# Optimization experiments

Hardware: AMD Instinct MI355X
Metric: run time of the kernel (lower is better)

Reference implementation:

```python
import jax, jax.numpy as jnp
import numpy as np

K = 3
PAD = 1
KK = K * K
GROUPS = 32  # min(32, dim) with dim=64
EPS = 1e-5


def _conv(x, w, pad):
    return jax.lax.conv_general_dilated(
        x, w, (1, 1), [(pad, pad), (pad, pad)],
        dimension_numbers=('NCHW', 'OIHW', 'NCHW'))


def _bilinear_gather(x, py, px):
    # x: (B,C,H,W); py,px: (B,KK,H,W) float sampling coords (zero pad outside)
    B, C, H, W = x.shape
    xf = x.reshape(B, C, H * W)
    y0f = jnp.floor(py)
    x0f = jnp.floor(px)
    wy1 = py - y0f  # fractional weights (differentiable path to offsets)
    wx1 = px - x0f
    y0 = y0f.astype(jnp.int32)
    x0 = x0f.astype(jnp.int32)

    def g(yi, xi):
        valid = (yi >= 0) & (yi < H) & (xi >= 0) & (xi < W)
        idx = (jnp.clip(yi, 0, H - 1) * W + jnp.clip(xi, 0, W - 1)).reshape(B, 1, -1)
        v = jnp.take_along_axis(xf, idx, axis=2).reshape(B, C, KK, H, W)
        return v * valid[:, None].astype(x.dtype)

    v00 = g(y0, x0)
    v01 = g(y0, x0 + 1)
    v10 = g(y0 + 1, x0)
    v11 = g(y0 + 1, x0 + 1)
    wy1e = wy1[:, None]
    wx1e = wx1[:, None]
    return (v00 * (1 - wy1e) * (1 - wx1e) + v01 * (1 - wy1e) * wx1e
            + v10 * wy1e * (1 - wx1e) + v11 * wy1e * wx1e)


def _forward(x, w_off1, w_off2, w_mask1, w_mask2, weight, bias, gamma, beta):
    B, C, H, W = x.shape
    # offset branch: 1x1 conv then KxK conv -> (B, 2*KK, H, W)
    off = _conv(_conv(x, w_off1, 0), w_off2, PAD).reshape(B, KK, 2, H, W)
    # mask branch -> sigmoid modulation (B, KK, H, W)
    mask = jax.nn.sigmoid(_conv(_conv(x, w_mask1, 0), w_mask2, PAD))
    # base kernel grid (torchvision deform_conv2d: pairs are (dy, dx) per tap)
    ky = jnp.repeat(jnp.arange(K) - PAD, K).astype(x.dtype)
    kx = jnp.tile(jnp.arange(K) - PAD, K).astype(x.dtype)
    py = off[:, :, 0] + jnp.arange(H, dtype=x.dtype)[None, None, :, None] + ky[None, :, None, None]
    px = off[:, :, 1] + jnp.arange(W, dtype=x.dtype)[None, None, None, :] + kx[None, :, None, None]
    samp = _bilinear_gather(x, py, px)  # (B, C, KK, H, W)
    # depthwise deformable conv: per-channel weight over KK taps, modulated by mask
    out = jnp.einsum('bkhw,ck,bckhw->bchw', mask, weight.reshape(C, KK), samp)
    out = out + bias[None, :, None, None]
    # GroupNorm(32, C)
    g = out.reshape(B, GROUPS, C // GROUPS, H, W)
    mu = g.mean(axis=(2, 3, 4), keepdims=True)
    var = g.var(axis=(2, 3, 4), keepdims=True)
    gn = ((g - mu) * jax.lax.rsqrt(var + EPS)).reshape(B, C, H, W)
    gn = gn * gamma[None, :, None, None] + beta[None, :, None, None]
    return jax.nn.gelu(gn, approximate=False)


def setup_inputs() -> dict:
    key = jax.random.key(0)
    ks = jax.random.split(key, 6)
    B, C, H, W = 4, 64, 128, 128
    x = jax.random.normal(ks[0], (B, C, H, W), dtype=jnp.float32)
    w_off1 = jax.random.normal(ks[1], (C, C, 1, 1), dtype=jnp.float32) * 0.05
    w_off2 = jax.random.normal(ks[2], (2 * KK, C, K, K), dtype=jnp.float32) * 0.02
    w_mask1 = jax.random.normal(ks[3], (C, C, 1, 1), dtype=jnp.float32) * 0.05
    w_mask2 = jax.random.normal(ks[4], (KK, C, K, K), dtype=jnp.float32) * 0.05
    bound = 1.0 / np.sqrt(KK)  # kaiming_uniform(a=1) for (C,1,K,K) -> fan_in=KK
    weight = jax.random.uniform(ks[5], (C, 1, K, K), dtype=jnp.float32,
                                minval=-bound, maxval=bound)
    bias = jnp.zeros((C,), dtype=jnp.float32)
    gamma = jnp.ones((C,), dtype=jnp.float32)
    beta = jnp.zeros((C,), dtype=jnp.float32)
    return {'x': x, 'w_off1': w_off1, 'w_off2': w_off2, 'w_mask1': w_mask1,
            'w_mask2': w_mask2, 'weight': weight, 'bias': bias,
            'gamma': gamma, 'beta': beta}


def reference(x, w_off1, w_off2, w_mask1, w_mask2, weight, bias, gamma, beta):
    return _forward(x, w_off1, w_off2, w_mask1, w_mask2, weight, bias, gamma, beta)
```

## Files before the change

kernel.cpp:

```cpp
#include <hip/hip_runtime.h>
#include <math.h>

#define B_  4
#define C_  64
#define H_  128
#define W_  128
#define HW_ (H_*W_)
#define NPIX_ (B_*HW_)
#define GROUPS_ 32

typedef __attribute__((ext_vector_type(8))) short short8;
typedef __attribute__((ext_vector_type(4))) float f32x4;

__device__ inline short f2bf_rne(float f) {
    unsigned u = __float_as_uint(f);
    unsigned r = (u + 0x7FFFu + ((u >> 16) & 1u)) >> 16;
    return (short)r;
}
__device__ inline float bf2f(short h) {
    return __uint_as_float(((unsigned)(unsigned short)h) << 16);
}
__device__ inline short8 ld8(const short* p) {
    union { uint4 u; short8 s; } c;
    c.u = *(const uint4*)p;
    return c.s;
}

__global__ void k0_prep(const float* __restrict__ w_off1, const float* __restrict__ w_mask1,
                        const float* __restrict__ w_off2, const float* __restrict__ w_mask2,
                        short* __restrict__ wc_hi, short* __restrict__ wc_lo) {
    int i = blockIdx.x * 256 + threadIdx.x;
    if (i >= 32 * 576) return;
    int cout = i / 576;
    int r    = i % 576;
    int pos  = r >> 6, ci = r & 63;
    float s = 0.f;
    if (cout < 18) {
        for (int cm = 0; cm < 64; cm++)
            s += w_off2[(cout * 64 + cm) * 9 + pos] * w_off1[cm * 64 + ci];
    } else if (cout < 27) {
        for (int cm = 0; cm < 64; cm++)
            s += w_mask2[((cout - 18) * 64 + cm) * 9 + pos] * w_mask1[cm * 64 + ci];
    }
    short h = f2bf_rne(s);
    wc_hi[i] = h;
    wc_lo[i] = f2bf_rne(s - bf2f(h));
}

__global__ __launch_bounds__(256) void k1_trans(const float* __restrict__ x,
                                                short* __restrict__ xtb) {
    int l   = threadIdx.x & 63;
    int wv  = threadIdx.x >> 6;
    int row = l >> 4, col = l & 15;
    int p0  = blockIdx.x * 64 + wv * 16;
    int b   = p0 >> 14;
    int hw  = p0 & (HW_ - 1);
    const float* xb = x + (size_t)b * C_ * HW_ + hw;
#pragma unroll
    for (int kb = 0; kb < 2; kb++) {
        int ci0 = kb * 32 + row * 8;
        float xv[8];
#pragma unroll
        for (int j = 0; j < 8; j++) xv[j] = xb[(ci0 + j) * HW_ + col];
        short8 a;
#pragma unroll
        for (int j = 0; j < 8; j++) a[j] = f2bf_rne(xv[j]);
        union { short8 s; uint4 u; } cv; cv.s = a;
        *(uint4*)(xtb + ((size_t)(p0 + col)) * 64 + ci0) = cv.u;
    }
}

__global__ __launch_bounds__(256, 2) void k2_mfma(const short* __restrict__ xtb,
                                                  const short* __restrict__ wc_hi,
                                                  const short* __restrict__ wc_lo,
                                                  float* __restrict__ offmask) {
    int l   = threadIdx.x & 63;
    int wv  = threadIdx.x >> 6;
    int row = l >> 4, col = l & 15;
    int blk = blockIdx.x;
    int h   = blk & 127;
    int pb  = blk * 128 + wv * 32;
    int w0  = (pb & 127);

    const short8 zero = {0,0,0,0,0,0,0,0};
    f32x4 a00 = {0.f,0.f,0.f,0.f};
    f32x4 a01 = {0.f,0.f,0.f,0.f};
    f32x4 a10 = {0.f,0.f,0.f,0.f};
    f32x4 a11 = {0.f,0.f,0.f,0.f};

    short8 cw0, cw1, cw2, cw3, ca0, ca1;
    {
        const int kb = 0, pos = 0, dy = -1, dx = -1;
        int ci0 = (kb & 1) * 32 + row * 8;
        int ko  = pos * 64 + ci0;
        cw0 = ld8(wc_hi + (size_t)col * 576 + ko);
        cw1 = ld8(wc_lo + (size_t)col * 576 + ko);
        cw2 = ld8(wc_hi + (size_t)(col + 16) * 576 + ko);
        cw3 = ld8(wc_lo + (size_t)(col + 16) * 576 + ko);
#pragma unroll
        for (int mt = 0; mt < 2; mt++) {
            int pbase = pb + mt * 16 + col;
            int w = w0 + mt * 16 + col;
            bool valid = ((unsigned)(h + dy) < 128u) && ((unsigned)(w + dx) < 128u);
            int addr = valid ? (pbase + dy * 128 + dx) : pbase;
            short8 v = ld8(xtb + (size_t)addr * 64 + ci0);
            if (mt == 0) ca0 = valid ? v : zero; else ca1 = valid ? v : zero;
        }
    }

#pragma unroll
    for (int kb = 0; kb < 18; kb++) {
        short8 nw0, nw1, nw2, nw3, na0, na1;
        if (kb < 17) {
            const int kn = kb + 1;
            const int pos = kn >> 1;
            const int dy = pos / 3 - 1, dx = pos % 3 - 1;
            int ci0 = (kn & 1) * 32 + row * 8;
            int ko  = pos * 64 + ci0;
            nw0 = ld8(wc_hi + (size_t)col * 576 + ko);
            nw1 = ld8(wc_lo + (size_t)col * 576 + ko);
            nw2 = ld8(wc_hi + (size_t)(col + 16) * 576 + ko);
            nw3 = ld8(wc_lo + (size_t)(col + 16) * 576 + ko);
#pragma unroll
            for (int mt = 0; mt < 2; mt++) {
                int pbase = pb + mt * 16 + col;
                int w = w0 + mt * 16 + col;
                bool valid = ((unsigned)(h + dy) < 128u) && ((unsigned)(w + dx) < 128u);
                int addr = valid ? (pbase + dy * 128 + dx) : pbase;
                short8 v = ld8(xtb + (size_t)addr * 64 + ci0);
                if (mt == 0) na0 = valid ? v : zero; else na1 = valid ? v : zero;
            }
        }
        a00 = __builtin_amdgcn_mfma_f32_16x16x32_bf16(ca0, cw0, a00, 0, 0, 0);
        a00 = __builtin_amdgcn_mfma_f32_16x16x32_bf16(ca0, cw1, a00, 0, 0, 0);
        a01 = __builtin_amdgcn_mfma_f32_16x16x32_bf16(ca0, cw2, a01, 0, 0, 0);
        a01 = __builtin_amdgcn_mfma_f32_16x16x32_bf16(ca0, cw3, a01, 0, 0, 0);
        a10 = __builtin_amdgcn_mfma_f32_16x16x32_bf16(ca1, cw0, a10, 0, 0, 0);
        a10 = __builtin_amdgcn_mfma_f32_16x16x32_bf16(ca1, cw1, a10, 0, 0, 0);
        a11 = __builtin_amdgcn_mfma_f32_16x16x32_bf16(ca1, cw2, a11, 0, 0, 0);
        a11 = __builtin_amdgcn_mfma_f32_16x16x32_bf16(ca1, cw3, a11, 0, 0, 0);
        cw0 = nw0; cw1 = nw1; cw2 = nw2; cw3 = nw3;
        ca0 = na0; ca1 = na1;
    }

#pragma unroll
    for (int mt = 0; mt < 2; mt++) {
        f32x4 n0 = mt ? a10 : a00;
        f32x4 n1 = mt ? a11 : a01;
#pragma unroll
        for (int r = 0; r < 4; r++) {
            int p = pb + mt * 16 + row * 4 + r;
            float* om = offmask + (size_t)p * 32;
            om[col] = n0[r];
            if (col < 2)       om[16 + col] = n1[r];
            else if (col < 11) om[16 + col] = 1.f / (1.f + expf(-n1[r]));
        }
    }
}

__global__ __launch_bounds__(256) void k3_deform(const short* __restrict__ xtb,
                                                 const float* __restrict__ offmask,
                                                 const float* __restrict__ weight,
                                                 const float* __restrict__ bias,
                                                 float* __restrict__ out_pre) {
    __shared__ float wl[C_ * 9];
    __shared__ float bl[C_];
    for (int i = threadIdx.x; i < C_ * 9; i += 256) wl[i] = weight[i];
    if (threadIdx.x < C_) bl[threadIdx.x] = bias[threadIdx.x];
    __syncthreads();

    int blk   = blockIdx.x;
    int xcd   = blk & 7;
    int slot  = blk >> 3;
    int b     = slot >> 5;
    int r     = (slot & 31) >> 1;
    int hrow  = slot & 1;
    int h     = xcd * 16 + r;
    int pl    = threadIdx.x >> 2;
    int chunk = threadIdx.x & 3;
    int c0    = chunk * 16;
    int w     = hrow * 64 + pl;
    int hw    = h * W_ + w;
    int P     = b * HW_ + hw;

    float acc[16];
#pragma unroll
    for (int i = 0; i < 16; i++) acc[i] = 0.f;

    const float* po = offmask + (size_t)P * 32;
    const short* xb = xtb + (size_t)b * HW_ * 64;

    for (int k = 0; k < 9; k++) {
        float offy = po[2 * k];
        float offx = po[2 * k + 1];
        float mk   = po[18 + k];
        float py = offy + (float)h + (float)(k / 3 - 1);
        float px = offx + (float)w + (float)(k % 3 - 1);
        float y0f = floorf(py), x0f = floorf(px);
        int y0 = (int)y0f, x0 = (int)x0f;
        int y1 = y0 + 1,   x1 = x0 + 1;
        float wy1 = py - y0f, wx1 = px - x0f;
        float wy0 = 1.f - wy1, wx0 = 1.f - wx1;
        bool vy0 = ((unsigned)y0 < (unsigned)H_);
        bool vy1 = ((unsigned)y1 < (unsigned)H_);
        bool vx0 = ((unsigned)x0 < (unsigned)W_);
        bool vx1 = ((unsigned)x1 < (unsigned)W_);
        int cy0 = min(max(y0, 0), H_ - 1);
        int cy1 = min(max(y1, 0), H_ - 1);
        int cx0 = min(max(x0, 0), W_ - 1);
        int cx1 = min(max(x1, 0), W_ - 1);
        float b00 = wy0 * wx0 * ((vy0 && vx0) ? mk : 0.f);
        float b01 = wy0 * wx1 * ((vy0 && vx1) ? mk : 0.f);
        float b10 = wy1 * wx0 * ((vy1 && vx0) ? mk : 0.f);
        float b11 = wy1 * wx1 * ((vy1 && vx1) ? mk : 0.f);

        const short* p00 = xb + ((size_t)cy0 * W_ + cx0) * 64 + c0;
        const short* p01 = xb + ((size_t)cy0 * W_ + cx1) * 64 + c0;
        const short* p10 = xb + ((size_t)cy1 * W_ + cx0) * 64 + c0;
        const short* p11 = xb + ((size_t)cy1 * W_ + cx1) * 64 + c0;

#pragma unroll
        for (int half = 0; half < 2; half++) {
            uint4 u00 = *(const uint4*)(p00 + 8 * half);
            uint4 u01 = *(const uint4*)(p01 + 8 * half);
            uint4 u10 = *(const uint4*)(p10 + 8 * half);
            uint4 u11 = *(const uint4*)(p11 + 8 * half);
            unsigned a00[4] = {u00.x, u00.y, u00.z, u00.w};
            unsigned a01[4] = {u01.x, u01.y, u01.z, u01.w};
            unsigned a10[4] = {u10.x, u10.y, u10.z, u10.w};
            unsigned a11[4] = {u11.x, u11.y, u11.z, u11.w};
#pragma unroll
            for (int d = 0; d < 4; d++) {
                float s_lo = b00 * __uint_as_float(a00[d] << 16)
                           + b01 * __uint_as_float(a01[d] << 16)
                           + b10 * __uint_as_float(a10[d] << 16)
                           + b11 * __uint_as_float(a11[d] << 16);
                float s_hi = b00 * __uint_as_float(a00[d] & 0xFFFF0000u)
                           + b01 * __uint_as_float(a01[d] & 0xFFFF0000u)
                           + b10 * __uint_as_float(a10[d] & 0xFFFF0000u)
                           + b11 * __uint_as_float(a11[d] & 0xFFFF0000u);
                int c = 8 * half + 2 * d;
                acc[c]     += wl[(c0 + c) * 9 + k] * s_lo;
                acc[c + 1] += wl[(c0 + c + 1) * 9 + k] * s_hi;
            }
        }
    }

    float* op = out_pre + ((size_t)b * C_ + c0) * HW_ + hw;
#pragma unroll
    for (int c = 0; c < 16; c++) op[c * HW_] = acc[c] + bl[c0 + c];
}

__global__ __launch_bounds__(1024) void k4_stats(const float* __restrict__ out_pre,
                                                 float* __restrict__ stats) {
    int bg = blockIdx.x;
    const float4* p = (const float4*)(out_pre + (size_t)bg * 2 * HW_);
    float s = 0.f, ss = 0.f;
    for (int i = threadIdx.x; i < 2 * HW_ / 4; i += 1024) {
        float4 v = p[i];
        s  += v.x + v.y + v.z + v.w;
        ss += v.x * v.x + v.y * v.y + v.z * v.z + v.w * v.w;
    }
#pragma unroll
    for (int m = 1; m < 64; m <<= 1) {
        s  += __shfl_xor(s, m);
        ss += __shfl_xor(ss, m);
    }
    __shared__ float ls[32];
    int lane = threadIdx.x & 63, wid = threadIdx.x >> 6;
    if (lane == 0) { ls[wid] = s; ls[16 + wid] = ss; }
    __syncthreads();
    if (threadIdx.x == 0) {
        float S = 0.f, SS = 0.f;
#pragma unroll
        for (int i = 0; i < 16; i++) { S += ls[i]; SS += ls[16 + i]; }
        const float inv = 1.f / (2.f * HW_);
        float mean = S * inv;
        float var  = SS * inv - mean * mean;
        stats[bg * 2]     = mean;
        stats[bg * 2 + 1] = rsqrtf(var + 1e-5f);
    }
}

__global__ __launch_bounds__(256) void k5_norm_gelu(const float* __restrict__ out_pre,
                                                    const float* __restrict__ stats,
                                                    const float* __restrict__ gamma,
                                                    const float* __restrict__ beta,
                                                    float* __restrict__ out) {
    int i = blockIdx.x * 256 + threadIdx.x;
    int e = i << 2;
    int c = (e >> 14) & (C_ - 1);
    int b = e >> 20;
    int bg = b * GROUPS_ + (c >> 1);
    float mean = stats[bg * 2];
    float rstd = stats[bg * 2 + 1];
    float ga = gamma[c] * rstd;
    float be = beta[c] - mean * ga;
    float4 v = ((const float4*)out_pre)[i];
    float4 r;
    float t;
    t = v.x * ga + be; r.x = 0.5f * t * (1.f + erff(t * 0.70710678118654752f));
    t = v.y * ga + be; r.y = 0.5f * t * (1.f + erff(t * 0.70710678118654752f));
    t = v.z * ga + be; r.z = 0.5f * t * (1.f + erff(t * 0.70710678118654752f));
    t = v.w * ga + be; r.w = 0.5f * t * (1.f + erff(t * 0.70710678118654752f));
    ((float4*)out)[i] = r;
}

extern "C" void kernel_launch(void* const* d_in, const int* in_sizes, int n_in,
                              void* d_out, int out_size, void* d_ws, size_t ws_size,
                              hipStream_t stream) {
    const float* x       = (const float*)d_in[0];
    const float* w_off1  = (const float*)d_in[1];
    const float* w_off2  = (const float*)d_in[2];
    const float* w_mask1 = (const float*)d_in[3];
    const float* w_mask2 = (const float*)d_in[4];
    const float* weight  = (const float*)d_in[5];
    const float* bias    = (const float*)d_in[6];
    const float* gamma   = (const float*)d_in[7];
    const float* beta    = (const float*)d_in[8];
    float* out = (float*)d_out;

    char* ws = (char*)d_ws;
    size_t o = 0;
    short* wc_hi = (short*)(ws + o); o += 32 * 576 * 2;
    short* wc_lo = (short*)(ws + o); o += 32 * 576 * 2;
    o = (o + 255) & ~(size_t)255;
    short* xtb     = (short*)(ws + o); o += (size_t)NPIX_ * 64 * 2;
    float* offmask = (float*)(ws + o); o += (size_t)NPIX_ * 32 * 4;
    float* out_pre = (float*)(ws + o); o += (size_t)NPIX_ * 64 * 4;
    float* stats   = (float*)(ws + o); o += 256 * 4;

    hipLaunchKernelGGL(k0_prep, dim3(72), dim3(256), 0, stream,
                       w_off1, w_mask1, w_off2, w_mask2, wc_hi, wc_lo);
    hipLaunchKernelGGL(k1_trans, dim3(NPIX_ / 64), dim3(256), 0, stream,
                       x, xtb);
    hipLaunchKernelGGL(k2_mfma, dim3(NPIX_ / 128), dim3(256), 0, stream,
                       xtb, wc_hi, wc_lo, offmask);
    hipLaunchKernelGGL(k3_deform, dim3(NPIX_ / 64), dim3(256), 0, stream,
                       xtb, offmask, weight, bias, out_pre);
    hipLaunchKernelGGL(k4_stats, dim3(B_ * GROUPS_), dim3(1024), 0, stream,
                       out_pre, stats);
    hipLaunchKernelGGL(k5_norm_gelu, dim3(NPIX_ * 64 / 4 / 256), dim3(256), 0, stream,
                       out_pre, stats, gamma, beta, out);
}
```

Measured before the change: 149.4 us.

## Fuse GroupNorm partial stats into deform kernel and store intermediate as bf16

The deformable-conv kernel now computes per-group sum and sum-of-squares partials through wavefront shuffles and LDS, so the stats kernel only reduces 256 partials per group instead of rereading the whole fp32 intermediate. The pre-norm intermediate is stored as bf16, which halves its write traffic and the read in the norm/GELU kernel, and that kernel now handles eight elements per thread. The cost is extra reduction work and a block barrier in the deform kernel, plus bf16 rounding of the pre-norm values before normalization, which may loosen accuracy.

```diff
diff --git a/kernel.cpp b/kernel.cpp
--- a/kernel.cpp
+++ b/kernel.cpp
@@ -90,8 +90,8 @@
 
     short8 cw0, cw1, cw2, cw3, ca0, ca1;
     {
-        const int kb = 0, pos = 0, dy = -1, dx = -1;
-        int ci0 = (kb & 1) * 32 + row * 8;
+        const int pos = 0, dy = -1, dx = -1;
+        int ci0 = row * 8;
         int ko  = pos * 64 + ci0;
         cw0 = ld8(wc_hi + (size_t)col * 576 + ko);
         cw1 = ld8(wc_lo + (size_t)col * 576 + ko);
@@ -162,9 +162,12 @@
                                                  const float* __restrict__ offmask,
                                                  const float* __restrict__ weight,
                                                  const float* __restrict__ bias,
-                                                 float* __restrict__ out_pre) {
+                                                 unsigned short* __restrict__ out_pre,
+                                                 float* __restrict__ partials) {
     __shared__ float wl[C_ * 9];
     __shared__ float bl[C_];
+    __shared__ float lds_s[4][4][8];
+    __shared__ float lds_ss[4][4][8];
     for (int i = threadIdx.x; i < C_ * 9; i += 256) wl[i] = weight[i];
     if (threadIdx.x < C_) bl[threadIdx.x] = bias[threadIdx.x];
     __syncthreads();
@@ -182,6 +185,7 @@
     int w     = hrow * 64 + pl;
     int hw    = h * W_ + w;
     int P     = b * HW_ + hw;
+    int slot_img = xcd * 32 + (slot & 31);
 
     float acc[16];
 #pragma unroll
@@ -246,34 +250,64 @@
         }
     }
 
-    float* op = out_pre + ((size_t)b * C_ + c0) * HW_ + hw;
-#pragma unroll
-    for (int c = 0; c < 16; c++) op[c * HW_] = acc[c] + bl[c0 + c];
-}
-
-__global__ __launch_bounds__(1024) void k4_stats(const float* __restrict__ out_pre,
+    unsigned short* op = out_pre + ((size_t)b * C_ + c0) * HW_ + hw;
+#pragma unroll
+    for (int c = 0; c < 16; c++) {
+        acc[c] += bl[c0 + c];
+        op[c * HW_] = (unsigned short)f2bf_rne(acc[c]);
+    }
+
+    float s8[8], ss8[8];
+#pragma unroll
+    for (int j = 0; j < 8; j++) {
+        float a0 = acc[2 * j], a1 = acc[2 * j + 1];
+        s8[j]  = a0 + a1;
+        ss8[j] = a0 * a0 + a1 * a1;
+    }
+#pragma unroll
+    for (int m = 4; m < 64; m <<= 1) {
+#pragma unroll
+        for (int j = 0; j < 8; j++) {
+            s8[j]  += __shfl_xor(s8[j], m);
+            ss8[j] += __shfl_xor(ss8[j], m);
+        }
+    }
+    int lane = threadIdx.x & 63, wid = threadIdx.x >> 6;
+    if (lane < 4) {
+#pragma unroll
+        for (int j = 0; j < 8; j++) {
+            lds_s[wid][lane][j]  = s8[j];
+            lds_ss[wid][lane][j] = ss8[j];
+        }
+    }
+    __syncthreads();
+    if (threadIdx.x < 32) {
+        int g = threadIdx.x;
+        int ch = g >> 3, j = g & 7;
+        float S  = lds_s[0][ch][j] + lds_s[1][ch][j] + lds_s[2][ch][j] + lds_s[3][ch][j];
+        float SS = lds_ss[0][ch][j] + lds_ss[1][ch][j] + lds_ss[2][ch][j] + lds_ss[3][ch][j];
+        float2 v = make_float2(S, SS);
+        *(float2*)(partials + (((size_t)(b * GROUPS_ + g)) * 256 + slot_img) * 2) = v;
+    }
+}
+
+__global__ __launch_bounds__(256) void k4_reduce(const float* __restrict__ partials,
                                                  float* __restrict__ stats) {
     int bg = blockIdx.x;
-    const float4* p = (const float4*)(out_pre + (size_t)bg * 2 * HW_);
-    float s = 0.f, ss = 0.f;
-    for (int i = threadIdx.x; i < 2 * HW_ / 4; i += 1024) {
-        float4 v = p[i];
-        s  += v.x + v.y + v.z + v.w;
-        ss += v.x * v.x + v.y * v.y + v.z * v.z + v.w * v.w;
-    }
+    float2 v = ((const float2*)partials)[bg * 256 + threadIdx.x];
+    float s = v.x, ss = v.y;
 #pragma unroll
     for (int m = 1; m < 64; m <<= 1) {
         s  += __shfl_xor(s, m);
         ss += __shfl_xor(ss, m);
     }
-    __shared__ float ls[32];
+    __shared__ float ls[8];
     int lane = threadIdx.x & 63, wid = threadIdx.x >> 6;
-    if (lane == 0) { ls[wid] = s; ls[16 + wid] = ss; }
+    if (lane == 0) { ls[wid] = s; ls[4 + wid] = ss; }
     __syncthreads();
     if (threadIdx.x == 0) {
-        float S = 0.f, SS = 0.f;
-#pragma unroll
-        for (int i = 0; i < 16; i++) { S += ls[i]; SS += ls[16 + i]; }
+        float S  = ls[0] + ls[1] + ls[2] + ls[3];
+        float SS = ls[4] + ls[5] + ls[6] + ls[7];
         const float inv = 1.f / (2.f * HW_);
         float mean = S * inv;
         float var  = SS * inv - mean * mean;
@@ -282,13 +316,13 @@
     }
 }
 
-__global__ __launch_bounds__(256) void k5_norm_gelu(const float* __restrict__ out_pre,
+__global__ __launch_bounds__(256) void k5_norm_gelu(const unsigned short* __restrict__ out_pre,
                                                     const float* __restrict__ stats,
                                                     const float* __restrict__ gamma,
                                                     const float* __restrict__ beta,
                                                     float* __restrict__ out) {
     int i = blockIdx.x * 256 + threadIdx.x;
-    int e = i << 2;
+    int e = i << 3;
     int c = (e >> 14) & (C_ - 1);
     int b = e >> 20;
     int bg = b * GROUPS_ + (c >> 1);
@@ -296,14 +330,23 @@
     float rstd = stats[bg * 2 + 1];
     float ga = gamma[c] * rstd;
     float be = beta[c] - mean * ga;
-    float4 v = ((const float4*)out_pre)[i];
-    float4 r;
-    float t;
-    t = v.x * ga + be; r.x = 0.5f * t * (1.f + erff(t * 0.70710678118654752f));
-    t = v.y * ga + be; r.y = 0.5f * t * (1.f + erff(t * 0.70710678118654752f));
-    t = v.z * ga + be; r.z = 0.5f * t * (1.f + erff(t * 0.70710678118654752f));
-    t = v.w * ga + be; r.w = 0.5f * t * (1.f + erff(t * 0.70710678118654752f));
-    ((float4*)out)[i] = r;
+    uint4 v = ((const uint4*)out_pre)[i];
+    unsigned dw[4] = {v.x, v.y, v.z, v.w};
+    float4 r0, r1;
+    float o[8];
+#pragma unroll
+    for (int d = 0; d < 4; d++) {
+        float lo = __uint_as_float(dw[d] << 16);
+        float hi = __uint_as_float(dw[d] & 0xFFFF0000u);
+        float t0 = lo * ga + be;
+        float t1 = hi * ga + be;
+        o[2 * d]     = 0.5f * t0 * (1.f + erff(t0 * 0.70710678118654752f));
+        o[2 * d + 1] = 0.5f * t1 * (1.f + erff(t1 * 0.70710678118654752f));
+    }
+    r0 = make_float4(o[0], o[1], o[2], o[3]);
+    r1 = make_float4(o[4], o[5], o[6], o[7]);
+    ((float4*)out)[2 * i]     = r0;
+    ((float4*)out)[2 * i + 1] = r1;
 }
 
 extern "C" void kernel_launch(void* const* d_in, const int* in_sizes, int n_in,
@@ -325,10 +368,11 @@
     short* wc_hi = (short*)(ws + o); o += 32 * 576 * 2;
     short* wc_lo = (short*)(ws + o); o += 32 * 576 * 2;
     o = (o + 255) & ~(size_t)255;
-    short* xtb     = (short*)(ws + o); o += (size_t)NPIX_ * 64 * 2;
-    float* offmask = (float*)(ws + o); o += (size_t)NPIX_ * 32 * 4;
-    float* out_pre = (float*)(ws + o); o += (size_t)NPIX_ * 64 * 4;
-    float* stats   = (float*)(ws + o); o += 256 * 4;
+    short* xtb               = (short*)(ws + o);          o += (size_t)NPIX_ * 64 * 2;
+    float* offmask           = (float*)(ws + o);          o += (size_t)NPIX_ * 32 * 4;
+    unsigned short* out_pre  = (unsigned short*)(ws + o); o += (size_t)NPIX_ * 64 * 2;
+    float* partials          = (float*)(ws + o);          o += (size_t)128 * 256 * 2 * 4;
+    float* stats             = (float*)(ws + o);          o += 256 * 4;
 
     hipLaunchKernelGGL(k0_prep, dim3(72), dim3(256), 0, stream,
                        w_off1, w_mask1, w_off2, w_mask2, wc_hi, wc_lo);
@@ -337,9 +381,9 @@
     hipLaunchKernelGGL(k2_mfma, dim3(NPIX_ / 128), dim3(256), 0, stream,
                        xtb, wc_hi, wc_lo, offmask);
     hipLaunchKernelGGL(k3_deform, dim3(NPIX_ / 64), dim3(256), 0, stream,
-                       xtb, offmask, weight, bias, out_pre);
-    hipLaunchKernelGGL(k4_stats, dim3(B_ * GROUPS_), dim3(1024), 0, stream,
-                       out_pre, stats);
-    hipLaunchKernelGGL(k5_norm_gelu, dim3(NPIX_ * 64 / 4 / 256), dim3(256), 0, stream,
+                       xtb, offmask, weight, bias, out_pre, partials);
+    hipLaunchKernelGGL(k4_reduce, dim3(B_ * GROUPS_), dim3(256), 0, stream,
+                       partials, stats);
+    hipLaunchKernelGGL(k5_norm_gelu, dim3(NPIX_ * 64 / 8 / 256), dim3(256), 0, stream,
                        out_pre, stats, gamma, beta, out);
 }
```

After: 146.0 us. 2.3% less time.
